# Kernel optimization log

Measured on AMD Instinct MI355X. Metric: run time of the kernel, lower is better.

Reference implementation:

```python
import jax, jax.numpy as jnp
import numpy as np

B, N1, N2, E = 128, 128, 384, 1024
N = N1 + N2
D_IN, D_FC = 64, 128
NUM_HEADS = 8.0  # args.num_att_heads
THETA = 1.0      # args.al_scale


def setup_inputs() -> dict:
    key = jax.random.key(0)
    ks = jax.random.split(key, 14)
    c_hs = jax.random.normal(ks[0], (B, N, D_IN), jnp.float32)
    attention = jax.random.uniform(ks[1], (B, N1, N2), jnp.float32)
    coords = jax.random.normal(ks[2], (B, N, 3), jnp.float32)
    upd_coords = coords + 0.1 * jax.random.normal(ks[3], (B, N, 3), jnp.float32)
    c_valid = jnp.ones((B, N), jnp.float32)
    nm = (jax.random.uniform(ks[4], (B, N1)) < 0.7).astype(jnp.float32)
    mapping = (jax.random.uniform(ks[5], (B, N, N)) < 0.05).astype(jnp.float32)
    samelb = jnp.maximum(mapping, (jax.random.uniform(ks[6], (B, N, N)) < 0.1).astype(jnp.float32))
    edge_index = jax.random.randint(ks[7], (B, E, 2), 0, N1, jnp.int32)
    W0 = jax.random.normal(ks[8], (D_IN, D_FC), jnp.float32) * 0.05
    b0 = jnp.zeros((D_FC,), jnp.float32)
    W1 = jax.random.normal(ks[9], (D_FC, D_FC), jnp.float32) * 0.05
    b1 = jnp.zeros((D_FC,), jnp.float32)
    W2 = jax.random.normal(ks[10], (D_FC, D_FC), jnp.float32) * 0.05
    b2 = jnp.zeros((D_FC,), jnp.float32)
    W3 = jax.random.normal(ks[11], (D_FC, 1), jnp.float32) * 0.05
    b3 = jnp.zeros((1,), jnp.float32)
    return dict(c_hs=c_hs, attention=attention, coords=coords, upd_coords=upd_coords,
                c_valid=c_valid, nm=nm, mapping=mapping, samelb=samelb,
                edge_index=edge_index, W0=W0, b0=b0, W1=W1, b1=b1, W2=W2, b2=b2, W3=W3, b3=b3)


def _kabsch(P, Q, m):
    # P, Q: [N1, 3], m: [N1] 0/1 non-modified mask
    Pm = P.mean(0)
    Qm = Q.mean(0)
    h = (P - Pm).T @ (Q - Qm) / NUM_HEADS  # [3,3]
    u, s, vt = jnp.linalg.svd(h)
    d = jnp.sign(jnp.linalg.det(h))
    corr = jnp.diag(jnp.concatenate([jnp.ones((2,), h.dtype), d[None].astype(h.dtype)]))
    r = u @ corr @ vt
    trans = Qm - r @ Pm
    Pp = P @ r.T + trans
    mk = (m > 0.5).astype(P.dtype)[:, None]
    cnt = jnp.maximum(mk.sum() * 3.0, 1.0)
    new_rmsd = (mk * (Pp - Q) ** 2).sum() / cnt        # mse over selected rows
    cen = ((Pp.mean(0) - Qm) ** 2).mean()              # centroid mse
    return new_rmsd, cen


def reference(c_hs, attention, coords, upd_coords, c_valid, nm, mapping, samelb,
              edge_index, W0, b0, W1, b1, W2, b2, W3, b3):
    # --- segment-sum pooling (sum_var_parts) + divide by n1, then FC head ---
    pooled = (c_hs * c_valid[..., None]).sum(axis=1) / float(N1)   # [B, D_IN]
    h = jax.nn.relu(pooled @ W0 + b0)
    h = jax.nn.relu(h @ W1 + b1)
    h = jax.nn.relu(h @ W2 + b2)
    scores = jax.nn.sigmoid(h @ W3 + b3).reshape(-1)               # [B]

    # --- cal_atten_batch + F.normalize(dim=1) ---
    atten = jnp.zeros((B, N, N), c_hs.dtype)
    atten = atten.at[:, :N1, N1:].set(attention)
    atten = atten.at[:, N1:, :N1].set(jnp.swapaxes(attention, 1, 2))
    nrm = jnp.sqrt((atten ** 2).sum(axis=1, keepdims=True))
    atten = atten / jnp.maximum(nrm, 1e-12)

    # --- cal_attn_loss ---
    top = jnp.where(mapping == 1.0, jnp.exp(-(atten * mapping)), 0.0).sum(axis=(1, 2))
    topabot = jnp.where(samelb == 1.0, jnp.exp(-(atten * samelb)), 0.0).sum(axis=(1, 2))
    attn_loss = (top / (topabot - top + 1.0)).sum() * THETA / float(B)

    # --- cal_rmsd_loss: straight-through one-hot mapping + Kabsch/SVD ---
    PP = upd_coords[:, :N1]   # subgraph updated coords
    QQ = coords[:, N1:]       # target graph original coords
    oh = jax.nn.one_hot(jnp.argmax(attention, axis=-1), N2, dtype=attention.dtype)
    st = oh + attention - jax.lax.stop_gradient(attention)         # straight-through
    Qsel = jnp.einsum('bij,bjd->bid', st, QQ)                      # [B, N1, 3]
    new_rmsd, cen = jax.vmap(_kabsch)(PP, Qsel, nm)
    rmsd_loss = new_rmsd.mean()
    centroid_loss = cen.mean()

    # --- cal_pairdst_loss over subgraph edges ---
    sub_c = coords[:, :N1]
    sub_u = upd_coords[:, :N1]
    bidx = jnp.arange(B)[:, None]
    d0 = jnp.sqrt(((sub_c[bidx, edge_index[..., 0]] - sub_c[bidx, edge_index[..., 1]]) ** 2).sum(-1) + 1e-12)
    d1 = jnp.sqrt(((sub_u[bidx, edge_index[..., 0]] - sub_u[bidx, edge_index[..., 1]]) ** 2).sum(-1) + 1e-12)
    pairdst_loss = jnp.abs((d1 - d0).sum(axis=-1)).mean()

    return scores, attn_loss, rmsd_loss, pairdst_loss, centroid_loss
```

## Files before the change

### kernel.cpp

```cpp
#include <hip/hip_runtime.h>
#include <math.h>

#define B_   128
#define N1_  128
#define N2_  384
#define N_   512
#define E_   1024
#define DIN  64
#define DFC  128

#define ACC_TOP  0
#define ACC_BOT  128
#define POOL_OFF 256
#define RN_OFF   (POOL_OFF + B_*DIN)
#define CN_OFF   (RN_OFF + B_*N1_)
#define BI_OFF   (CN_OFF + B_*N2_)
#define ZERO_CNT (POOL_OFF + B_*DIN)

__global__ void k_init(float* ws, float* out) {
    int idx = blockIdx.x * 256 + threadIdx.x;
    if (idx < ZERO_CNT) ws[idx] = 0.f;
    if (blockIdx.x == 0 && threadIdx.x < 4) out[128 + threadIdx.x] = 0.f;
}

__global__ void k_pool(const float* __restrict__ c_hs, const float* __restrict__ c_valid,
                       float* __restrict__ ws) {
    __shared__ float4 sred[256];
    int b = blockIdx.x, t = threadIdx.x;
    int chunk = blockIdx.y * 64;
    int d4 = t & 15, rl = t >> 4;
    const float4* X4 = (const float4*)(c_hs + (size_t)b * N_ * DIN);
    const float* V = c_valid + (size_t)b * N_;
    float4 acc = {0.f, 0.f, 0.f, 0.f};
    #pragma unroll
    for (int r = chunk + rl; r < chunk + 64; r += 16) {
        float4 x = X4[r * 16 + d4];
        float v = V[r];
        acc.x += x.x * v; acc.y += x.y * v; acc.z += x.z * v; acc.w += x.w * v;
    }
    sred[t] = acc; __syncthreads();
    for (int off = 128; off >= 16; off >>= 1) {
        if (t < off) {
            float4 o = sred[t + off];
            sred[t].x += o.x; sred[t].y += o.y; sred[t].z += o.z; sred[t].w += o.w;
        }
        __syncthreads();
    }
    if (t < 16) {
        float4 s = sred[t];
        float* p = ws + POOL_OFF + b * DIN + t * 4;
        atomicAdd(&p[0], s.x); atomicAdd(&p[1], s.y);
        atomicAdd(&p[2], s.z); atomicAdd(&p[3], s.w);
    }
}

__global__ void k_mlp2(const float* __restrict__ ws,
                       const float* __restrict__ W0, const float* __restrict__ b0,
                       const float* __restrict__ W1, const float* __restrict__ b1,
                       const float* __restrict__ W2, const float* __restrict__ b2,
                       const float* __restrict__ W3, const float* __restrict__ b3,
                       float* __restrict__ out) {
    __shared__ float pool[DIN];
    __shared__ float h[DFC];
    __shared__ float h2[DFC];
    __shared__ float part[DFC];
    int b = blockIdx.x, t = threadIdx.x;
    if (t < DIN) pool[t] = ws[POOL_OFF + b * DIN + t] * (1.0f / 128.0f);
    __syncthreads();
    float a = b0[t];
    for (int i = 0; i < DIN; ++i) a += pool[i] * W0[i * DFC + t];
    h[t] = fmaxf(a, 0.f); __syncthreads();
    a = b1[t];
    for (int i = 0; i < DFC; ++i) a += h[i] * W1[i * DFC + t];
    h2[t] = fmaxf(a, 0.f); __syncthreads();
    a = b2[t];
    for (int i = 0; i < DFC; ++i) a += h2[i] * W2[i * DFC + t];
    part[t] = fmaxf(a, 0.f) * W3[t];
    __syncthreads();
    for (int off = 64; off > 0; off >>= 1) { if (t < off) part[t] += part[t + off]; __syncthreads(); }
    if (t == 0) out[b] = 1.f / (1.f + expf(-(part[0] + b3[0])));
}

__global__ void k_rows(const float* __restrict__ att, float* __restrict__ ws) {
    int b = blockIdx.x, t = threadIdx.x, wv = t >> 6, ln = t & 63;
    int r = blockIdx.y * 4 + wv;
    const float* row = att + ((size_t)b * N1_ + r) * N2_;
    float ssq = 0.f, best = -1e30f; int bidx = 0;
    #pragma unroll
    for (int q = 0; q < 6; ++q) {
        float v = row[ln + 64 * q];
        ssq += v * v;
        if (v > best) { best = v; bidx = ln + 64 * q; }
    }
    for (int off = 32; off > 0; off >>= 1) {
        ssq += __shfl_xor(ssq, off, 64);
        float ov = __shfl_xor(best, off, 64);
        int oi = __shfl_xor(bidx, off, 64);
        if (ov > best || (ov == best && oi < bidx)) { best = ov; bidx = oi; }
    }
    if (ln == 0) {
        ws[RN_OFF + b * N1_ + r] = sqrtf(ssq);
        ((int*)ws)[BI_OFF + b * N1_ + r] = bidx;
    }
}

__global__ void k_cols(const float* __restrict__ att, float* __restrict__ ws) {
    __shared__ float sred[256];
    int b = blockIdx.x, t = threadIdx.x;
    int c = blockIdx.y * 128 + (t & 127);
    int half = t >> 7;
    const float* A = att + (size_t)b * N1_ * N2_;
    float s = 0.f;
    #pragma unroll 16
    for (int j = half * 64; j < half * 64 + 64; ++j) { float v = A[j * N2_ + c]; s += v * v; }
    sred[t] = s; __syncthreads();
    if (t < 128) ws[CN_OFF + b * N2_ + blockIdx.y * 128 + t] = sqrtf(sred[t] + sred[t + 128]);
}

__device__ inline float cnt4(float4 m) {
    return (m.x == 1.f ? 1.f : 0.f) + (m.y == 1.f ? 1.f : 0.f)
         + (m.z == 1.f ? 1.f : 0.f) + (m.w == 1.f ? 1.f : 0.f);
}

#define ASTR 388
__global__ void k_maskA(const float* __restrict__ att, const float* __restrict__ mapping,
                        const float* __restrict__ samelb, float* __restrict__ ws) {
    __shared__ float cninv[N2_];
    __shared__ float esh[16 * ASTR];
    __shared__ float rt[4], rb[4];
    int b = blockIdx.y, t = threadIdx.x;
    int i0 = blockIdx.x * 16;
    for (int j = t; j < N2_; j += 256)
        cninv[j] = 1.f / fmaxf(ws[CN_OFF + b * N2_ + j], 1e-12f);
    __syncthreads();
    const float4* att4 = (const float4*)(att + ((size_t)(b * N1_ + i0)) * N2_);
    #pragma unroll
    for (int k = 0; k < 6; ++k) {
        int f = t + k * 256;
        int r = f / 96, c4 = f - r * 96;
        float4 a = att4[r * 96 + c4];
        int cb = c4 * 4;
        esh[r * ASTR + cb]     = __expf(-a.x * cninv[cb]);
        esh[r * ASTR + cb + 1] = __expf(-a.y * cninv[cb + 1]);
        esh[r * ASTR + cb + 2] = __expf(-a.z * cninv[cb + 2]);
        esh[r * ASTR + cb + 3] = __expf(-a.w * cninv[cb + 3]);
    }
    __syncthreads();
    const float4* m4 = (const float4*)(mapping + ((size_t)b * N_ + i0) * N_);
    const float4* s4 = (const float4*)(samelb + ((size_t)b * N_ + i0) * N_);
    float top = 0.f, bot = 0.f;
    #pragma unroll
    for (int k = 0; k < 2; ++k) {
        int g = t + k * 256; int r = g >> 5, c4 = g & 31;
        top += cnt4(m4[r * 128 + c4]);
        bot += cnt4(s4[r * 128 + c4]);
    }
    #pragma unroll
    for (int k = 0; k < 6; ++k) {
        int g = t + k * 256; int r = g / 96, c4 = g - r * 96;
        float4 mv = m4[r * 128 + 32 + c4];
        float4 sv = s4[r * 128 + 32 + c4];
        int eb = r * ASTR + c4 * 4;
        float e0 = esh[eb], e1 = esh[eb + 1], e2 = esh[eb + 2], e3 = esh[eb + 3];
        top += (mv.x == 1.f ? e0 : 0.f) + (mv.y == 1.f ? e1 : 0.f)
             + (mv.z == 1.f ? e2 : 0.f) + (mv.w == 1.f ? e3 : 0.f);
        bot += (sv.x == 1.f ? e0 : 0.f) + (sv.y == 1.f ? e1 : 0.f)
             + (sv.z == 1.f ? e2 : 0.f) + (sv.w == 1.f ? e3 : 0.f);
    }
    for (int off = 32; off > 0; off >>= 1) {
        top += __shfl_down(top, off, 64);
        bot += __shfl_down(bot, off, 64);
    }
    int wv = t >> 6, ln = t & 63;
    if (ln == 0) { rt[wv] = top; rb[wv] = bot; }
    __syncthreads();
    if (t == 0) {
        atomicAdd(&ws[ACC_TOP + b], rt[0] + rt[1] + rt[2] + rt[3]);
        atomicAdd(&ws[ACC_BOT + b], rb[0] + rb[1] + rb[2] + rb[3]);
    }
}

#define BSTR 132
__global__ void k_maskB(const float* __restrict__ att, const float* __restrict__ mapping,
                        const float* __restrict__ samelb, float* __restrict__ ws) {
    __shared__ float rinv[N1_];
    __shared__ float tile[16 * BSTR];
    __shared__ float rt[4], rb[4];
    int b = blockIdx.y, t = threadIdx.x;
    int k0 = blockIdx.x * 16;
    if (t < N1_) rinv[t] = 1.f / fmaxf(ws[RN_OFF + b * N1_ + t], 1e-12f);
    __syncthreads();
    int r4 = t & 3;
    for (int j = (t >> 2); j < N1_; j += 64) {
        float4 a = *(const float4*)&att[((size_t)(b * N1_ + j)) * N2_ + k0 + r4 * 4];
        float rv = rinv[j];
        tile[(r4 * 4 + 0) * BSTR + j] = __expf(-a.x * rv);
        tile[(r4 * 4 + 1) * BSTR + j] = __expf(-a.y * rv);
        tile[(r4 * 4 + 2) * BSTR + j] = __expf(-a.z * rv);
        tile[(r4 * 4 + 3) * BSTR + j] = __expf(-a.w * rv);
    }
    __syncthreads();
    const float4* m4 = (const float4*)(mapping + ((size_t)b * N_ + N1_ + k0) * N_);
    const float4* s4 = (const float4*)(samelb + ((size_t)b * N_ + N1_ + k0) * N_);
    float top = 0.f, bot = 0.f;
    #pragma unroll
    for (int k = 0; k < 2; ++k) {
        int g = t + k * 256; int r = g >> 5, c4 = g & 31;
        float4 mv = m4[r * 128 + c4];
        float4 sv = s4[r * 128 + c4];
        int eb = r * BSTR + c4 * 4;
        float e0 = tile[eb], e1 = tile[eb + 1], e2 = tile[eb + 2], e3 = tile[eb + 3];
        top += (mv.x == 1.f ? e0 : 0.f) + (mv.y == 1.f ? e1 : 0.f)
             + (mv.z == 1.f ? e2 : 0.f) + (mv.w == 1.f ? e3 : 0.f);
        bot += (sv.x == 1.f ? e0 : 0.f) + (sv.y == 1.f ? e1 : 0.f)
             + (sv.z == 1.f ? e2 : 0.f) + (sv.w == 1.f ? e3 : 0.f);
    }
    #pragma unroll
    for (int k = 0; k < 6; ++k) {
        int g = t + k * 256; int r = g / 96, c4 = g - r * 96;
        top += cnt4(m4[r * 128 + 32 + c4]);
        bot += cnt4(s4[r * 128 + 32 + c4]);
    }
    for (int off = 32; off > 0; off >>= 1) {
        top += __shfl_down(top, off, 64);
        bot += __shfl_down(bot, off, 64);
    }
    int wv = t >> 6, ln = t & 63;
    if (ln == 0) { rt[wv] = top; rb[wv] = bot; }
    __syncthreads();
    if (t == 0) {
        atomicAdd(&ws[ACC_TOP + b], rt[0] + rt[1] + rt[2] + rt[3]);
        atomicAdd(&ws[ACC_BOT + b], rb[0] + rb[1] + rb[2] + rb[3]);
    }
}

__device__ inline float bred(float* s, float v, int t) {
    __syncthreads();
    s[t] = v; __syncthreads();
    for (int off = 64; off > 0; off >>= 1) { if (t < off) s[t] += s[t + off]; __syncthreads(); }
    float r = s[0]; __syncthreads(); return r;
}

__global__ void k_kabsch(const float* __restrict__ coords, const float* __restrict__ upd,
                         const float* __restrict__ nm, const int* __restrict__ ei,
                         const float* __restrict__ ws, float* __restrict__ out) {
    __shared__ float sred[128];
    __shared__ float Rsh[9], Tsh[3];
    int b = blockIdx.x, t = threadIdx.x;
    int bidx = ((const int*)ws)[BI_OFF + b * N1_ + t];
    float P[3], Q[3];
    const float* up = upd + ((size_t)b * N_ + t) * 3;
    P[0] = up[0]; P[1] = up[1]; P[2] = up[2];
    const float* qp = coords + ((size_t)b * N_ + N1_ + bidx) * 3;
    Q[0] = qp[0]; Q[1] = qp[1]; Q[2] = qp[2];
    float Pm[3], Qm[3];
    for (int a = 0; a < 3; ++a) Pm[a] = bred(sred, P[a], t) * (1.f / 128.f);
    for (int a = 0; a < 3; ++a) Qm[a] = bred(sred, Q[a], t) * (1.f / 128.f);
    float H[9];
    for (int a = 0; a < 3; ++a)
        for (int c = 0; c < 3; ++c)
            H[a * 3 + c] = bred(sred, (P[a] - Pm[a]) * (Q[c] - Qm[c]), t) * (1.f / 8.f);
    if (t == 0) {
        double Hd[3][3];
        for (int a = 0; a < 3; ++a) for (int c = 0; c < 3; ++c) Hd[a][c] = (double)H[a * 3 + c];
        double A[3][3], V[3][3] = {{1,0,0},{0,1,0},{0,0,1}};
        for (int i = 0; i < 3; ++i)
            for (int j = 0; j < 3; ++j) {
                double s2 = 0; for (int c = 0; c < 3; ++c) s2 += Hd[c][i] * Hd[c][j];
                A[i][j] = s2;
            }
        for (int sweep = 0; sweep < 12; ++sweep) {
            const int PQ[3][2] = {{0,1},{0,2},{1,2}};
            for (int r = 0; r < 3; ++r) {
                int p = PQ[r][0], q = PQ[r][1];
                double apq = A[p][q];
                if (fabs(apq) < 1e-300) continue;
                double tau = (A[q][q] - A[p][p]) / (2.0 * apq);
                double tt = (tau >= 0 ? 1.0 : -1.0) / (fabs(tau) + sqrt(1.0 + tau * tau));
                double c = 1.0 / sqrt(1.0 + tt * tt), s = tt * c;
                for (int k = 0; k < 3; ++k) { double akp = A[k][p], akq = A[k][q]; A[k][p] = c * akp - s * akq; A[k][q] = s * akp + c * akq; }
                for (int k = 0; k < 3; ++k) { double apk = A[p][k], aqk = A[q][k]; A[p][k] = c * apk - s * aqk; A[q][k] = s * apk + c * aqk; }
                for (int k = 0; k < 3; ++k) { double vkp = V[k][p], vkq = V[k][q]; V[k][p] = c * vkp - s * vkq; V[k][q] = s * vkp + c * vkq; }
            }
        }
        double lam[3] = {A[0][0], A[1][1], A[2][2]};
        int id[3] = {0, 1, 2};
        if (lam[id[0]] < lam[id[1]]) { int x = id[0]; id[0] = id[1]; id[1] = x; }
        if (lam[id[0]] < lam[id[2]]) { int x = id[0]; id[0] = id[2]; id[2] = x; }
        if (lam[id[1]] < lam[id[2]]) { int x = id[1]; id[1] = id[2]; id[2] = x; }
        double u[3][3], v[3][3], sv[3];
        for (int i = 0; i < 3; ++i) {
            for (int k = 0; k < 3; ++k) v[i][k] = V[k][id[i]];
            double uv[3];
            for (int c = 0; c < 3; ++c) uv[c] = Hd[c][0] * v[i][0] + Hd[c][1] * v[i][1] + Hd[c][2] * v[i][2];
            double n = sqrt(uv[0] * uv[0] + uv[1] * uv[1] + uv[2] * uv[2]);
            sv[i] = n;
            if (n > 1e-150) { u[i][0] = uv[0] / n; u[i][1] = uv[1] / n; u[i][2] = uv[2] / n; }
            else { u[i][0] = u[i][1] = u[i][2] = 0.0; }
        }
        if (sv[2] < 1e-12 * fmax(sv[0], 1e-300)) {
            u[2][0] = u[0][1] * u[1][2] - u[0][2] * u[1][1];
            u[2][1] = u[0][2] * u[1][0] - u[0][0] * u[1][2];
            u[2][2] = u[0][0] * u[1][1] - u[0][1] * u[1][0];
        }
        double det = Hd[0][0] * (Hd[1][1] * Hd[2][2] - Hd[1][2] * Hd[2][1])
                   - Hd[0][1] * (Hd[1][0] * Hd[2][2] - Hd[1][2] * Hd[2][0])
                   + Hd[0][2] * (Hd[1][0] * Hd[2][1] - Hd[1][1] * Hd[2][0]);
        double dsg = (det > 0.0) ? 1.0 : ((det < 0.0) ? -1.0 : 0.0);
        for (int a = 0; a < 3; ++a)
            for (int c = 0; c < 3; ++c)
                Rsh[a * 3 + c] = (float)(u[0][a] * v[0][c] + u[1][a] * v[1][c] + dsg * u[2][a] * v[2][c]);
        for (int a = 0; a < 3; ++a)
            Tsh[a] = Qm[a] - (Rsh[a * 3] * Pm[0] + Rsh[a * 3 + 1] * Pm[1] + Rsh[a * 3 + 2] * Pm[2]);
    }
    __syncthreads();
    float Pp[3];
    for (int a = 0; a < 3; ++a)
        Pp[a] = Rsh[a * 3] * P[0] + Rsh[a * 3 + 1] * P[1] + Rsh[a * 3 + 2] * P[2] + Tsh[a];
    float mk = (nm[b * N1_ + t] > 0.5f) ? 1.f : 0.f;
    float dx = Pp[0] - Q[0], dy = Pp[1] - Q[1], dz = Pp[2] - Q[2];
    float rsum = bred(sred, mk * (dx * dx + dy * dy + dz * dz), t);
    float msum = bred(sred, mk, t);
    float Ppm[3];
    for (int a = 0; a < 3; ++a) Ppm[a] = bred(sred, Pp[a], t) * (1.f / 128.f);
    if (t == 0) {
        float cnt = fmaxf(msum * 3.f, 1.f);
        atomicAdd(&out[129], (rsum / cnt) * (1.f / 128.f));
        float cen = 0.f;
        for (int a = 0; a < 3; ++a) { float d2 = Ppm[a] - Qm[a]; cen += d2 * d2; }
        atomicAdd(&out[131], (cen / 3.f) * (1.f / 128.f));
    }
    const float* C = coords + (size_t)b * N_ * 3;
    const float* U = upd + (size_t)b * N_ * 3;
    const int* e = ei + (size_t)b * E_ * 2;
    float acc = 0.f;
    for (int idx = t; idx < E_; idx += 128) {
        int a0 = e[idx * 2], a1 = e[idx * 2 + 1];
        float ex = C[a0 * 3] - C[a1 * 3], ey = C[a0 * 3 + 1] - C[a1 * 3 + 1], ez = C[a0 * 3 + 2] - C[a1 * 3 + 2];
        float d0 = sqrtf(ex * ex + ey * ey + ez * ez + 1e-12f);
        ex = U[a0 * 3] - U[a1 * 3]; ey = U[a0 * 3 + 1] - U[a1 * 3 + 1]; ez = U[a0 * 3 + 2] - U[a1 * 3 + 2];
        float d1 = sqrtf(ex * ex + ey * ey + ez * ez + 1e-12f);
        acc += d1 - d0;
    }
    float psum = bred(sred, acc, t);
    if (t == 0) atomicAdd(&out[130], fabsf(psum) * (1.f / 128.f));
    if (b == 0) {
        float top = ws[ACC_TOP + t], bot = ws[ACC_BOT + t];
        float v = top / (bot - top + 1.0f);
        float s = bred(sred, v, t);
        if (t == 0) out[128] = s * (1.0f / 128.0f);
    }
}

extern "C" void kernel_launch(void* const* d_in, const int* in_sizes, int n_in,
                              void* d_out, int out_size, void* d_ws, size_t ws_size,
                              hipStream_t stream) {
    const float* c_hs      = (const float*)d_in[0];
    const float* attention = (const float*)d_in[1];
    const float* coords    = (const float*)d_in[2];
    const float* upd       = (const float*)d_in[3];
    const float* c_valid   = (const float*)d_in[4];
    const float* nm        = (const float*)d_in[5];
    const float* mapping   = (const float*)d_in[6];
    const float* samelb    = (const float*)d_in[7];
    const int*   ei        = (const int*)d_in[8];
    const float* W0 = (const float*)d_in[9],  *b0 = (const float*)d_in[10];
    const float* W1 = (const float*)d_in[11], *b1 = (const float*)d_in[12];
    const float* W2 = (const float*)d_in[13], *b2 = (const float*)d_in[14];
    const float* W3 = (const float*)d_in[15], *b3 = (const float*)d_in[16];
    float* out = (float*)d_out;
    float* ws  = (float*)d_ws;

    hipLaunchKernelGGL(k_init,   dim3(33),      dim3(256), 0, stream, ws, out);
    hipLaunchKernelGGL(k_pool,   dim3(B_, 8),   dim3(256), 0, stream, c_hs, c_valid, ws);
    hipLaunchKernelGGL(k_mlp2,   dim3(B_),      dim3(DFC), 0, stream, ws,
                       W0, b0, W1, b1, W2, b2, W3, b3, out);
    hipLaunchKernelGGL(k_rows,   dim3(B_, 32),  dim3(256), 0, stream, attention, ws);
    hipLaunchKernelGGL(k_cols,   dim3(B_, 3),   dim3(256), 0, stream, attention, ws);
    hipLaunchKernelGGL(k_maskA,  dim3(8, B_),   dim3(256), 0, stream, attention, mapping, samelb, ws);
    hipLaunchKernelGGL(k_maskB,  dim3(24, B_),  dim3(256), 0, stream, attention, mapping, samelb, ws);
    hipLaunchKernelGGL(k_kabsch, dim3(B_),      dim3(N1_), 0, stream, coords, upd, nm, ei, ws, out);
}
```

Before: 403.3 us.

## Merge mask kernels into one scan, precompute transposed exp tile, trim reductions

```diff
diff --git a/kernel.cpp b/kernel.cpp
--- a/kernel.cpp
+++ b/kernel.cpp
@@ -12,9 +12,10 @@
 #define ACC_TOP  0
 #define ACC_BOT  128
 #define POOL_OFF 256
-#define RN_OFF   (POOL_OFF + B_*DIN)
-#define CN_OFF   (RN_OFF + B_*N1_)
-#define BI_OFF   (CN_OFF + B_*N2_)
+#define RNI_OFF  (POOL_OFF + B_*DIN)
+#define CNI_OFF  (RNI_OFF + B_*N1_)
+#define BI_OFF   (CNI_OFF + B_*N2_)
+#define EB_OFF   (BI_OFF + B_*N1_)
 #define ZERO_CNT (POOL_OFF + B_*DIN)
 
 __global__ void k_init(float* ws, float* out) {
@@ -68,12 +69,15 @@
     if (t < DIN) pool[t] = ws[POOL_OFF + b * DIN + t] * (1.0f / 128.0f);
     __syncthreads();
     float a = b0[t];
+    #pragma unroll
     for (int i = 0; i < DIN; ++i) a += pool[i] * W0[i * DFC + t];
     h[t] = fmaxf(a, 0.f); __syncthreads();
     a = b1[t];
+    #pragma unroll
     for (int i = 0; i < DFC; ++i) a += h[i] * W1[i * DFC + t];
     h2[t] = fmaxf(a, 0.f); __syncthreads();
     a = b2[t];
+    #pragma unroll
     for (int i = 0; i < DFC; ++i) a += h2[i] * W2[i * DFC + t];
     part[t] = fmaxf(a, 0.f) * W3[t];
     __syncthreads();
@@ -99,7 +103,7 @@
         if (ov > best || (ov == best && oi < bidx)) { best = ov; bidx = oi; }
     }
     if (ln == 0) {
-        ws[RN_OFF + b * N1_ + r] = sqrtf(ssq);
+        ws[RNI_OFF + b * N1_ + r] = 1.f / fmaxf(sqrtf(ssq), 1e-12f);
         ((int*)ws)[BI_OFF + b * N1_ + r] = bidx;
     }
 }
@@ -107,14 +111,51 @@
 __global__ void k_cols(const float* __restrict__ att, float* __restrict__ ws) {
     __shared__ float sred[256];
     int b = blockIdx.x, t = threadIdx.x;
-    int c = blockIdx.y * 128 + (t & 127);
-    int half = t >> 7;
+    int c = blockIdx.y * 64 + (t & 63);
+    int q = t >> 6;
     const float* A = att + (size_t)b * N1_ * N2_;
     float s = 0.f;
-    #pragma unroll 16
-    for (int j = half * 64; j < half * 64 + 64; ++j) { float v = A[j * N2_ + c]; s += v * v; }
+    #pragma unroll 8
+    for (int j = q * 32; j < q * 32 + 32; ++j) { float v = A[j * N2_ + c]; s += v * v; }
     sred[t] = s; __syncthreads();
-    if (t < 128) ws[CN_OFF + b * N2_ + blockIdx.y * 128 + t] = sqrtf(sred[t] + sred[t + 128]);
+    if (t < 64)
+        ws[CNI_OFF + b * N2_ + blockIdx.y * 64 + t] =
+            1.f / fmaxf(sqrtf(sred[t] + sred[t + 64] + sred[t + 128] + sred[t + 192]), 1e-12f);
+}
+
+#define TP 129
+__global__ void k_prep(const float* __restrict__ att, float* __restrict__ ws) {
+    __shared__ float tile[32 * TP];
+    __shared__ float rinv[N1_];
+    int b = blockIdx.y, t = threadIdx.x;
+    int r0 = blockIdx.x * 32;
+    if (t < N1_) rinv[t] = ws[RNI_OFF + b * N1_ + t];
+    __syncthreads();
+    const float4* att4 = (const float4*)(att + (size_t)b * N1_ * N2_);
+    int c8 = t & 7, jb = t >> 3;
+    #pragma unroll
+    for (int p = 0; p < 4; ++p) {
+        int j = jb + p * 32;
+        float4 a = att4[j * 96 + blockIdx.x * 8 + c8];
+        float rv = rinv[j];
+        tile[(c8 * 4 + 0) * TP + j] = a.x * rv;
+        tile[(c8 * 4 + 1) * TP + j] = a.y * rv;
+        tile[(c8 * 4 + 2) * TP + j] = a.z * rv;
+        tile[(c8 * 4 + 3) * TP + j] = a.w * rv;
+    }
+    __syncthreads();
+    int j4 = t & 31, cb = t >> 5;
+    float4* eb4 = (float4*)(ws + EB_OFF + ((size_t)b * N2_ + r0) * N1_);
+    #pragma unroll
+    for (int p = 0; p < 4; ++p) {
+        int c = cb + p * 8;
+        float4 e;
+        e.x = __expf(-tile[c * TP + j4 * 4]);
+        e.y = __expf(-tile[c * TP + j4 * 4 + 1]);
+        e.z = __expf(-tile[c * TP + j4 * 4 + 2]);
+        e.w = __expf(-tile[c * TP + j4 * 4 + 3]);
+        eb4[c * 32 + j4] = e;
+    }
 }
 
 __device__ inline float cnt4(float4 m) {
@@ -122,50 +163,60 @@
          + (m.z == 1.f ? 1.f : 0.f) + (m.w == 1.f ? 1.f : 0.f);
 }
 
-#define ASTR 388
-__global__ void k_maskA(const float* __restrict__ att, const float* __restrict__ mapping,
-                        const float* __restrict__ samelb, float* __restrict__ ws) {
+__global__ void k_scan(const float* __restrict__ att, const float* __restrict__ mapping,
+                       const float* __restrict__ samelb, float* __restrict__ ws) {
     __shared__ float cninv[N2_];
-    __shared__ float esh[16 * ASTR];
     __shared__ float rt[4], rb[4];
     int b = blockIdx.y, t = threadIdx.x;
     int i0 = blockIdx.x * 16;
-    for (int j = t; j < N2_; j += 256)
-        cninv[j] = 1.f / fmaxf(ws[CN_OFF + b * N2_ + j], 1e-12f);
-    __syncthreads();
-    const float4* att4 = (const float4*)(att + ((size_t)(b * N1_ + i0)) * N2_);
-    #pragma unroll
-    for (int k = 0; k < 6; ++k) {
-        int f = t + k * 256;
-        int r = f / 96, c4 = f - r * 96;
-        float4 a = att4[r * 96 + c4];
-        int cb = c4 * 4;
-        esh[r * ASTR + cb]     = __expf(-a.x * cninv[cb]);
-        esh[r * ASTR + cb + 1] = __expf(-a.y * cninv[cb + 1]);
-        esh[r * ASTR + cb + 2] = __expf(-a.z * cninv[cb + 2]);
-        esh[r * ASTR + cb + 3] = __expf(-a.w * cninv[cb + 3]);
-    }
-    __syncthreads();
     const float4* m4 = (const float4*)(mapping + ((size_t)b * N_ + i0) * N_);
     const float4* s4 = (const float4*)(samelb + ((size_t)b * N_ + i0) * N_);
     float top = 0.f, bot = 0.f;
-    #pragma unroll
-    for (int k = 0; k < 2; ++k) {
-        int g = t + k * 256; int r = g >> 5, c4 = g & 31;
-        top += cnt4(m4[r * 128 + c4]);
-        bot += cnt4(s4[r * 128 + c4]);
-    }
-    #pragma unroll
-    for (int k = 0; k < 6; ++k) {
-        int g = t + k * 256; int r = g / 96, c4 = g - r * 96;
-        float4 mv = m4[r * 128 + 32 + c4];
-        float4 sv = s4[r * 128 + 32 + c4];
-        int eb = r * ASTR + c4 * 4;
-        float e0 = esh[eb], e1 = esh[eb + 1], e2 = esh[eb + 2], e3 = esh[eb + 3];
-        top += (mv.x == 1.f ? e0 : 0.f) + (mv.y == 1.f ? e1 : 0.f)
-             + (mv.z == 1.f ? e2 : 0.f) + (mv.w == 1.f ? e3 : 0.f);
-        bot += (sv.x == 1.f ? e0 : 0.f) + (sv.y == 1.f ? e1 : 0.f)
-             + (sv.z == 1.f ? e2 : 0.f) + (sv.w == 1.f ? e3 : 0.f);
+    if (i0 < N1_) {
+        for (int j = t; j < N2_; j += 256) cninv[j] = ws[CNI_OFF + b * N2_ + j];
+        __syncthreads();
+        #pragma unroll
+        for (int k = 0; k < 2; ++k) {
+            int g = t + k * 256; int r = g >> 5, c4 = g & 31;
+            top += cnt4(m4[r * 128 + c4]);
+            bot += cnt4(s4[r * 128 + c4]);
+        }
+        const float4* a4 = (const float4*)(att + ((size_t)b * N1_ + i0) * N2_);
+        #pragma unroll
+        for (int k = 0; k < 6; ++k) {
+            int g = t + k * 256; int r = g / 96, c4 = g - r * 96;
+            float4 mv = m4[r * 128 + 32 + c4];
+            float4 sv = s4[r * 128 + 32 + c4];
+            float4 a  = a4[r * 96 + c4];
+            int cb = c4 * 4;
+            float e0 = __expf(-a.x * cninv[cb]);
+            float e1 = __expf(-a.y * cninv[cb + 1]);
+            float e2 = __expf(-a.z * cninv[cb + 2]);
+            float e3 = __expf(-a.w * cninv[cb + 3]);
+            top += (mv.x == 1.f ? e0 : 0.f) + (mv.y == 1.f ? e1 : 0.f)
+                 + (mv.z == 1.f ? e2 : 0.f) + (mv.w == 1.f ? e3 : 0.f);
+            bot += (sv.x == 1.f ? e0 : 0.f) + (sv.y == 1.f ? e1 : 0.f)
+                 + (sv.z == 1.f ? e2 : 0.f) + (sv.w == 1.f ? e3 : 0.f);
+        }
+    } else {
+        const float4* eb4 = (const float4*)(ws + EB_OFF + ((size_t)b * N2_ + (i0 - N1_)) * N1_);
+        #pragma unroll
+        for (int k = 0; k < 2; ++k) {
+            int g = t + k * 256; int r = g >> 5, c4 = g & 31;
+            float4 mv = m4[r * 128 + c4];
+            float4 sv = s4[r * 128 + c4];
+            float4 e  = eb4[r * 32 + c4];
+            top += (mv.x == 1.f ? e.x : 0.f) + (mv.y == 1.f ? e.y : 0.f)
+                 + (mv.z == 1.f ? e.z : 0.f) + (mv.w == 1.f ? e.w : 0.f);
+            bot += (sv.x == 1.f ? e.x : 0.f) + (sv.y == 1.f ? e.y : 0.f)
+                 + (sv.z == 1.f ? e.z : 0.f) + (sv.w == 1.f ? e.w : 0.f);
+        }
+        #pragma unroll
+        for (int k = 0; k < 6; ++k) {
+            int g = t + k * 256; int r = g / 96, c4 = g - r * 96;
+            top += cnt4(m4[r * 128 + 32 + c4]);
+            bot += cnt4(s4[r * 128 + 32 + c4]);
+        }
     }
     for (int off = 32; off > 0; off >>= 1) {
         top += __shfl_down(top, off, 64);
@@ -180,71 +231,19 @@
     }
 }
 
-#define BSTR 132
-__global__ void k_maskB(const float* __restrict__ att, const float* __restrict__ mapping,
-                        const float* __restrict__ samelb, float* __restrict__ ws) {
-    __shared__ float rinv[N1_];
-    __shared__ float tile[16 * BSTR];
-    __shared__ float rt[4], rb[4];
-    int b = blockIdx.y, t = threadIdx.x;
-    int k0 = blockIdx.x * 16;
-    if (t < N1_) rinv[t] = 1.f / fmaxf(ws[RN_OFF + b * N1_ + t], 1e-12f);
-    __syncthreads();
-    int r4 = t & 3;
-    for (int j = (t >> 2); j < N1_; j += 64) {
-        float4 a = *(const float4*)&att[((size_t)(b * N1_ + j)) * N2_ + k0 + r4 * 4];
-        float rv = rinv[j];
-        tile[(r4 * 4 + 0) * BSTR + j] = __expf(-a.x * rv);
-        tile[(r4 * 4 + 1) * BSTR + j] = __expf(-a.y * rv);
-        tile[(r4 * 4 + 2) * BSTR + j] = __expf(-a.z * rv);
-        tile[(r4 * 4 + 3) * BSTR + j] = __expf(-a.w * rv);
-    }
-    __syncthreads();
-    const float4* m4 = (const float4*)(mapping + ((size_t)b * N_ + N1_ + k0) * N_);
-    const float4* s4 = (const float4*)(samelb + ((size_t)b * N_ + N1_ + k0) * N_);
-    float top = 0.f, bot = 0.f;
-    #pragma unroll
-    for (int k = 0; k < 2; ++k) {
-        int g = t + k * 256; int r = g >> 5, c4 = g & 31;
-        float4 mv = m4[r * 128 + c4];
-        float4 sv = s4[r * 128 + c4];
-        int eb = r * BSTR + c4 * 4;
-        float e0 = tile[eb], e1 = tile[eb + 1], e2 = tile[eb + 2], e3 = tile[eb + 3];
-        top += (mv.x == 1.f ? e0 : 0.f) + (mv.y == 1.f ? e1 : 0.f)
-             + (mv.z == 1.f ? e2 : 0.f) + (mv.w == 1.f ? e3 : 0.f);
-        bot += (sv.x == 1.f ? e0 : 0.f) + (sv.y == 1.f ? e1 : 0.f)
-             + (sv.z == 1.f ? e2 : 0.f) + (sv.w == 1.f ? e3 : 0.f);
-    }
-    #pragma unroll
-    for (int k = 0; k < 6; ++k) {
-        int g = t + k * 256; int r = g / 96, c4 = g - r * 96;
-        top += cnt4(m4[r * 128 + 32 + c4]);
-        bot += cnt4(s4[r * 128 + 32 + c4]);
-    }
-    for (int off = 32; off > 0; off >>= 1) {
-        top += __shfl_down(top, off, 64);
-        bot += __shfl_down(bot, off, 64);
-    }
-    int wv = t >> 6, ln = t & 63;
-    if (ln == 0) { rt[wv] = top; rb[wv] = bot; }
-    __syncthreads();
-    if (t == 0) {
-        atomicAdd(&ws[ACC_TOP + b], rt[0] + rt[1] + rt[2] + rt[3]);
-        atomicAdd(&ws[ACC_BOT + b], rb[0] + rb[1] + rb[2] + rb[3]);
-    }
-}
-
-__device__ inline float bred(float* s, float v, int t) {
-    __syncthreads();
-    s[t] = v; __syncthreads();
-    for (int off = 64; off > 0; off >>= 1) { if (t < off) s[t] += s[t + off]; __syncthreads(); }
-    float r = s[0]; __syncthreads(); return r;
+__device__ inline float bred(float* s2, float v, int t) {
+    for (int off = 32; off > 0; off >>= 1) v += __shfl_down(v, off, 64);
+    if ((t & 63) == 0) s2[t >> 6] = v;
+    __syncthreads();
+    float r = s2[0] + s2[1];
+    __syncthreads();
+    return r;
 }
 
 __global__ void k_kabsch(const float* __restrict__ coords, const float* __restrict__ upd,
                          const float* __restrict__ nm, const int* __restrict__ ei,
                          const float* __restrict__ ws, float* __restrict__ out) {
-    __shared__ float sred[128];
+    __shared__ float s2[2];
     __shared__ float Rsh[9], Tsh[3];
     int b = blockIdx.x, t = threadIdx.x;
     int bidx = ((const int*)ws)[BI_OFF + b * N1_ + t];
@@ -254,22 +253,22 @@
     const float* qp = coords + ((size_t)b * N_ + N1_ + bidx) * 3;
     Q[0] = qp[0]; Q[1] = qp[1]; Q[2] = qp[2];
     float Pm[3], Qm[3];
-    for (int a = 0; a < 3; ++a) Pm[a] = bred(sred, P[a], t) * (1.f / 128.f);
-    for (int a = 0; a < 3; ++a) Qm[a] = bred(sred, Q[a], t) * (1.f / 128.f);
+    for (int a = 0; a < 3; ++a) Pm[a] = bred(s2, P[a], t) * (1.f / 128.f);
+    for (int a = 0; a < 3; ++a) Qm[a] = bred(s2, Q[a], t) * (1.f / 128.f);
     float H[9];
     for (int a = 0; a < 3; ++a)
         for (int c = 0; c < 3; ++c)
-            H[a * 3 + c] = bred(sred, (P[a] - Pm[a]) * (Q[c] - Qm[c]), t) * (1.f / 8.f);
+            H[a * 3 + c] = bred(s2, (P[a] - Pm[a]) * (Q[c] - Qm[c]), t) * (1.f / 8.f);
     if (t == 0) {
         double Hd[3][3];
         for (int a = 0; a < 3; ++a) for (int c = 0; c < 3; ++c) Hd[a][c] = (double)H[a * 3 + c];
         double A[3][3], V[3][3] = {{1,0,0},{0,1,0},{0,0,1}};
         for (int i = 0; i < 3; ++i)
             for (int j = 0; j < 3; ++j) {
-                double s2 = 0; for (int c = 0; c < 3; ++c) s2 += Hd[c][i] * Hd[c][j];
-                A[i][j] = s2;
+                double z = 0; for (int c = 0; c < 3; ++c) z += Hd[c][i] * Hd[c][j];
+                A[i][j] = z;
             }
-        for (int sweep = 0; sweep < 12; ++sweep) {
+        for (int sweep = 0; sweep < 8; ++sweep) {
             const int PQ[3][2] = {{0,1},{0,2},{1,2}};
             for (int r = 0; r < 3; ++r) {
                 int p = PQ[r][0], q = PQ[r][1];
@@ -319,10 +318,10 @@
         Pp[a] = Rsh[a * 3] * P[0] + Rsh[a * 3 + 1] * P[1] + Rsh[a * 3 + 2] * P[2] + Tsh[a];
     float mk = (nm[b * N1_ + t] > 0.5f) ? 1.f : 0.f;
     float dx = Pp[0] - Q[0], dy = Pp[1] - Q[1], dz = Pp[2] - Q[2];
-    float rsum = bred(sred, mk * (dx * dx + dy * dy + dz * dz), t);
-    float msum = bred(sred, mk, t);
+    float rsum = bred(s2, mk * (dx * dx + dy * dy + dz * dz), t);
+    float msum = bred(s2, mk, t);
     float Ppm[3];
-    for (int a = 0; a < 3; ++a) Ppm[a] = bred(sred, Pp[a], t) * (1.f / 128.f);
+    for (int a = 0; a < 3; ++a) Ppm[a] = bred(s2, Pp[a], t) * (1.f / 128.f);
     if (t == 0) {
         float cnt = fmaxf(msum * 3.f, 1.f);
         atomicAdd(&out[129], (rsum / cnt) * (1.f / 128.f));
@@ -342,12 +341,12 @@
         float d1 = sqrtf(ex * ex + ey * ey + ez * ez + 1e-12f);
         acc += d1 - d0;
     }
-    float psum = bred(sred, acc, t);
+    float psum = bred(s2, acc, t);
     if (t == 0) atomicAdd(&out[130], fabsf(psum) * (1.f / 128.f));
     if (b == 0) {
         float top = ws[ACC_TOP + t], bot = ws[ACC_BOT + t];
         float v = top / (bot - top + 1.0f);
-        float s = bred(sred, v, t);
+        float s = bred(s2, v, t);
         if (t == 0) out[128] = s * (1.0f / 128.0f);
     }
 }
@@ -376,8 +375,8 @@
     hipLaunchKernelGGL(k_mlp2,   dim3(B_),      dim3(DFC), 0, stream, ws,
                        W0, b0, W1, b1, W2, b2, W3, b3, out);
     hipLaunchKernelGGL(k_rows,   dim3(B_, 32),  dim3(256), 0, stream, attention, ws);
-    hipLaunchKernelGGL(k_cols,   dim3(B_, 3),   dim3(256), 0, stream, attention, ws);
-    hipLaunchKernelGGL(k_maskA,  dim3(8, B_),   dim3(256), 0, stream, attention, mapping, samelb, ws);
-    hipLaunchKernelGGL(k_maskB,  dim3(24, B_),  dim3(256), 0, stream, attention, mapping, samelb, ws);
+    hipLaunchKernelGGL(k_cols,   dim3(B_, 6),   dim3(256), 0, stream, attention, ws);
+    hipLaunchKernelGGL(k_prep,   dim3(12, B_),  dim3(256), 0, stream, attention, ws);
+    hipLaunchKernelGGL(k_scan,   dim3(32, B_),  dim3(256), 0, stream, attention, mapping, samelb, ws);
     hipLaunchKernelGGL(k_kabsch, dim3(B_),      dim3(N1_), 0, stream, coords, upd, nm, ei, ws, out);
 }
```

After: 389.9 us. 1.03x faster.
